# Optimization experiments

Measured on AMD Instinct MI355X. Metric: run time of the kernel, lower is better.

The kernel has to match this reference:

```python
import jax, jax.numpy as jnp
import numpy as np

K = 5          # kernel_size per pseudo-coordinate dim
N_NODES = 50000
N_EDGES = 800000
N_GRAPHS = 128


def _spline_basis(pseudo):
    # degree-1 open B-spline basis in 2-D pseudo coordinates.
    v = jnp.clip(pseudo, 0.0, 1.0) * (K - 1)            # [E,2]
    k0 = jnp.clip(jnp.floor(v), 0, K - 2).astype(jnp.int32)  # [E,2]
    frac = v - k0.astype(v.dtype)                        # [E,2]
    return k0, frac


def _spline_conv(x, src, dst, k0, frac, weight, root, bias, n_nodes):
    # weight: [K*K, in, out]. Precompute per-node per-kernel transform
    # to avoid materializing per-edge [E,in,out] weights.
    x_k = jnp.einsum('ni,kio->nko', x, weight)           # [N, 25, out]
    out_dim = weight.shape[2]
    msg = jnp.zeros((src.shape[0], out_dim), dtype=x.dtype)
    for b0 in range(2):          # 2^dim = 4 contributing basis combos
        for b1 in range(2):
            basis = ((frac[:, 0] if b0 else 1.0 - frac[:, 0])
                     * (frac[:, 1] if b1 else 1.0 - frac[:, 1]))   # [E]
            idx = (k0[:, 0] + b0) * K + (k0[:, 1] + b1)            # [E]
            msg = msg + basis[:, None] * x_k[src, idx]             # gather [E,out]
    agg = jax.ops.segment_sum(msg, dst, num_segments=n_nodes)      # [N,out]
    deg = jax.ops.segment_sum(jnp.ones((src.shape[0],), x.dtype), dst,
                              num_segments=n_nodes)
    agg = agg / jnp.maximum(deg, 1.0)[:, None]                     # aggr='mean'
    return agg + x @ root + bias


def setup_inputs() -> dict:
    key = jax.random.key(0)
    ks = jax.random.split(key, 16)
    x = jax.random.normal(ks[0], (N_NODES, 8), dtype=jnp.float32)
    edge_index = jax.random.randint(ks[1], (2, N_EDGES), 0, N_NODES, dtype=jnp.int32)
    pseudo = jax.random.uniform(ks[2], (N_EDGES, 2), dtype=jnp.float32)
    batch = jnp.sort(jax.random.randint(ks[3], (N_NODES,), 0, N_GRAPHS, dtype=jnp.int32))
    s = 0.1
    w1 = s * jax.random.normal(ks[4], (K * K, 8, 32), dtype=jnp.float32)
    r1 = s * jax.random.normal(ks[5], (8, 32), dtype=jnp.float32)
    b1 = jnp.zeros((32,), jnp.float32)
    w2 = s * jax.random.normal(ks[6], (K * K, 32, 64), dtype=jnp.float32)
    r2 = s * jax.random.normal(ks[7], (32, 64), dtype=jnp.float32)
    b2 = jnp.zeros((64,), jnp.float32)
    w3 = s * jax.random.normal(ks[8], (K * K, 64, 64), dtype=jnp.float32)
    r3 = s * jax.random.normal(ks[9], (64, 64), dtype=jnp.float32)
    b3 = jnp.zeros((64,), jnp.float32)
    fc_w = s * jax.random.normal(ks[10], (64, 30), dtype=jnp.float32)
    fc_b = jnp.zeros((30,), jnp.float32)
    return dict(x=x, edge_index=edge_index, pseudo=pseudo, batch=batch,
                w1=w1, r1=r1, b1=b1, w2=w2, r2=r2, b2=b2, w3=w3, r3=r3, b3=b3,
                fc_w=fc_w, fc_b=fc_b)


def reference(x, edge_index, pseudo, batch, w1, r1, b1, w2, r2, b2, w3, r3, b3, fc_w, fc_b):
    src, dst = edge_index[0], edge_index[1]
    k0, frac = _spline_basis(pseudo)
    h = jax.nn.elu(_spline_conv(x, src, dst, k0, frac, w1, r1, b1, N_NODES))
    h = jax.nn.elu(_spline_conv(h, src, dst, k0, frac, w2, r2, b2, N_NODES))
    h = jax.nn.elu(_spline_conv(h, src, dst, k0, frac, w3, r3, b3, N_NODES))
    # scatter_mean pooling over graphs (data.batch)
    pooled = jax.ops.segment_sum(h, batch, num_segments=N_GRAPHS)
    cnt = jax.ops.segment_sum(jnp.ones((N_NODES,), h.dtype), batch,
                              num_segments=N_GRAPHS)
    pooled = pooled / jnp.maximum(cnt, 1.0)[:, None]     # [G,64]
    # dropout is identity at inference
    logits = pooled @ fc_w + fc_b                        # [G,30]
    return jax.nn.log_softmax(logits, axis=1)
```

## Files before the change

### kernel.cpp

```cpp
#include <hip/hip_runtime.h>
#include <hip/hip_bf16.h>
#include <math.h>


typedef __attribute__((ext_vector_type(8))) short bf16x8;
typedef __attribute__((ext_vector_type(4))) float f32x4;

constexpr int SCAN_CHUNK = 2048;

__device__ __forceinline__ unsigned short f2bf(float f) {
    union { float f; unsigned u; } v; v.f = f;
    return (unsigned short)((v.u + 0x7fffu + ((v.u >> 16) & 1u)) >> 16);
}
__device__ __forceinline__ float bf2f(unsigned short h) {
    union { unsigned u; float f; } v; v.u = ((unsigned)h) << 16;
    return v.f;
}
__device__ __forceinline__ int pairaddr(int kk) {
    int slice = kk >> 5;
    return (slice >> 1) * 72 + (slice & 1) * 32 + (kk & 31);
}


__global__ void hist_kernel(const int* __restrict__ ei, int* __restrict__ deg, int E) {
    int e = blockIdx.x * blockDim.x + threadIdx.x;
    if (e < E) atomicAdd(&deg[ei[E + e]], 1);
}

__global__ __launch_bounds__(256) void scan1_kernel(const int* __restrict__ deg,
                                                    int* __restrict__ blockSums, int n) {
    __shared__ int wsum[4];
    int tid = threadIdx.x, lane = tid & 63, wave = tid >> 6;
    int idx0 = blockIdx.x * SCAN_CHUNK + tid * 8;
    int s = 0;
    #pragma unroll
    for (int u = 0; u < 8; ++u) {
        int id = idx0 + u;
        int d = (id < n) ? deg[id] : 0;
        s += (d + 7) & ~7;
    }
    #pragma unroll
    for (int off = 1; off < 64; off <<= 1) s += __shfl_xor(s, off);
    if (lane == 0) wsum[wave] = s;
    __syncthreads();
    if (tid == 0) blockSums[blockIdx.x] = wsum[0] + wsum[1] + wsum[2] + wsum[3];
}

__global__ void scan2_kernel(int* __restrict__ blockSums, int* __restrict__ row_start,
                             int nb, int n) {
    int lane = threadIdx.x & 63;
    int v = (lane < nb) ? blockSums[lane] : 0;
    int inc = v;
    #pragma unroll
    for (int off = 1; off < 64; off <<= 1) {
        int t = __shfl_up(inc, off);
        if (lane >= off) inc += t;
    }
    if (lane < nb) blockSums[lane] = inc - v;
    if (lane == 63) row_start[n] = inc;
}

__global__ __launch_bounds__(256) void scan3_kernel(const int* __restrict__ deg,
                                                    const int* __restrict__ blockSums,
                                                    int* __restrict__ row_start,
                                                    int* __restrict__ cursor,
                                                    float* __restrict__ invdeg, int n) {
    __shared__ int wsum[4];
    int tid = threadIdx.x, lane = tid & 63, wave = tid >> 6;
    int carry = blockSums[blockIdx.x];
    int idx0 = blockIdx.x * SCAN_CHUNK + tid * 8;
    int v[8], pre[8];
    int s = 0;
    #pragma unroll
    for (int u = 0; u < 8; ++u) {
        int id = idx0 + u;
        int d = (id < n) ? deg[id] : 0;
        v[u] = d;
        pre[u] = s;
        s += (d + 7) & ~7;
    }
    int inc = s;
    #pragma unroll
    for (int off = 1; off < 64; off <<= 1) {
        int t = __shfl_up(inc, off);
        if (lane >= off) inc += t;
    }
    if (lane == 63) wsum[wave] = inc;
    __syncthreads();
    int woff = 0;
    for (int w2 = 0; w2 < wave; ++w2) woff += wsum[w2];
    int eb = carry + woff + inc - s;
    #pragma unroll
    for (int u = 0; u < 8; ++u) {
        int id = idx0 + u;
        if (id < n) {
            int rs = eb + pre[u];
            row_start[id] = rs;
            cursor[id] = rs;
            invdeg[id] = 1.0f / fmaxf((float)v[u], 1.0f);
        }
    }
}

__global__ void scatter_kernel(const int* __restrict__ ei, const float* __restrict__ pseudo,
                               const float* __restrict__ invdeg, int* __restrict__ cursor,
                               uint2* __restrict__ basisB, unsigned* __restrict__ metaB, int E) {
    int e = blockIdx.x * blockDim.x + threadIdx.x;
    if (e >= E) return;
    int src = ei[e], dst = ei[E + e];
    float p0 = pseudo[2 * e], p1 = pseudo[2 * e + 1];
    float v0 = fminf(fmaxf(p0, 0.f), 1.f) * 4.f;
    float v1 = fminf(fmaxf(p1, 0.f), 1.f) * 4.f;
    int k00 = min((int)floorf(v0), 3);
    int k01 = min((int)floorf(v1), 3);
    float f0 = v0 - (float)k00, f1 = v1 - (float)k01;
    float g0 = 1.f - f0, g1 = 1.f - f1;
    float sc = invdeg[dst];
    int i00 = k00 * 5 + k01;
    int pos = atomicAdd(&cursor[dst], 1);
    uint2 b;
    b.x = (unsigned)f2bf(g0 * g1 * sc) | ((unsigned)f2bf(g0 * f1 * sc) << 16);
    b.y = (unsigned)f2bf(f0 * g1 * sc) | ((unsigned)f2bf(f0 * f1 * sc) << 16);
    basisB[pos] = b;
    metaB[pos] = (unsigned)src | ((unsigned)i00 << 20);
}

template <int Cin, int Cout, int KW>
__global__ void wprep_kernel(const float* __restrict__ W, const float* __restrict__ root,
                             unsigned short* __restrict__ WtF) {
    constexpr int NT = Cout / 16;
    int idx = blockIdx.x * 256 + threadIdx.x;
    if (idx >= Cout * KW) return;
    int e = idx & 7;
    int lane = (idx >> 3) & 63;
    int sn = idx >> 9;
    int s = sn / NT, nt = sn - s * NT;
    int r16 = lane & 15, g8 = lane >> 4;
    int o = nt * 16 + r16;
    int kk = s * 32 + g8 * 8 + e;
    float v = 0.f;
    if (kk < 26 * Cin) {
        int k = kk / Cin, i = kk - k * Cin;
        v = (k < 25) ? W[(k * Cin + i) * Cout + o] : root[i * Cout + o];
    }
    WtF[idx] = f2bf(v);
}


template <int Cin, int Cout, bool F32IN>
__global__ __launch_bounds__(512, 4) void layer_kernel(
        const void* __restrict__ xin_, const unsigned short* __restrict__ WtF,
        const float* __restrict__ bias, const int* __restrict__ row_start,
        const int* __restrict__ row_end, const uint2* __restrict__ basisG,
        const unsigned* __restrict__ metaG, unsigned short* __restrict__ xout,
        int nNodes) {
    constexpr int T = 16;
    constexpr int SLICES = (26 * Cin + 31) / 32;
    constexpr int NPAIR = (SLICES + 1) / 2;
    constexpr int ST = NPAIR * 72 + 8;
    constexpr int MT = (Cin + 15) / 16;
    constexpr int NT_B = Cout / 16;
    constexpr int W8 = 8 / NT_B;
    constexpr int RS = Cout + 4;
    constexpr int BSZ = 32 * 34;
    constexpr int DEPTH = (MT <= 2) ? 2 : 1;

    __shared__ __align__(16) unsigned short acc[T * ST];
    __shared__ __align__(16) unsigned short Ball[8 * BSZ];

    const int tid = threadIdx.x;
    const int node0 = blockIdx.x * T;
    const int wave = tid >> 6, lane = tid & 63;
    const int r16 = lane & 15, g8 = lane >> 4;
    const float* xf = (const float*)xin_;
    const unsigned short* xb = (const unsigned short*)xin_;

    {
        uint4 z = make_uint4(0u, 0u, 0u, 0u);
        for (int p = tid; p < T * ST / 8; p += 512) ((uint4*)acc)[p] = z;
    }
    __syncthreads();
    for (int p = tid; p < T * Cin; p += 512) {
        int t = p / Cin, i = p - t * Cin;
        int n = node0 + t;
        if (n < nNodes) {
            unsigned short v = F32IN ? f2bf(xf[n * Cin + i]) : xb[n * Cin + i];
            acc[t * ST + pairaddr(25 * Cin + i)] = v;
        }
    }

    unsigned short* Bw = Ball + wave * BSZ;
    {
        const int t0 = wave, t1 = wave + 8;
        const int na = node0 + t0, nb = node0 + t1;
        int eb0 = 0, ee0 = 0, eb1 = 0, ee1 = 0;
        if (na < nNodes) { eb0 = row_start[na]; ee0 = row_end[na]; }
        if (nb < nNodes) { eb1 = row_start[nb]; ee1 = row_end[nb]; }
        const int nc0 = (ee0 - eb0 + 31) >> 5;
        const int nc1 = (ee1 - eb1 + 31) >> 5;
        const int TC = nc0 + nc1;

        if (TC > 0) {
            auto info = [&](int vc, int& base, int& ee) {
                bool first = vc < nc0;
                int c = first ? vc : vc - nc0;
                base = (first ? eb0 : eb1) + (c << 5);
                ee = first ? ee0 : ee1;
            };
            auto loadMeta = [&](int vc, uint4& a, uint4& b) {
                int base, ee;
                info(vc, base, ee);
                const uint4* p = (const uint4*)(metaG + base + g8 * 8);
                a = p[0];
                b = p[1];
            };
            auto gatherA = [&](const uint4& a, const uint4& b, bf16x8* af) {
                int s[8];
                s[0] = a.x & 0xFFFFF; s[1] = a.y & 0xFFFFF;
                s[2] = a.z & 0xFFFFF; s[3] = a.w & 0xFFFFF;
                s[4] = b.x & 0xFFFFF; s[5] = b.y & 0xFFFFF;
                s[6] = b.z & 0xFFFFF; s[7] = b.w & 0xFFFFF;
                #pragma unroll
                for (int mt = 0; mt < MT; ++mt) {
                    int col = (Cin >= 16) ? (mt * 16 + r16) : (r16 & (Cin - 1));
                    #pragma unroll
                    for (int j = 0; j < 8; ++j)
                        af[mt][j] = (short)(F32IN ? f2bf(xf[s[j] * Cin + col])
                                                  : xb[s[j] * Cin + col]);
                }
            };
            auto loadScat = [&](int vc, unsigned& bx, unsigned& by, int& i00,
                                bool& valid) {
                int base, ee;
                info(vc, base, ee);
                int e = base + (lane & 31);
                valid = (lane < 32) && (e < ee);
                uint2 bb = basisG[e];
                unsigned mm = metaG[e];
                bx = bb.x;
                by = bb.y;
                i00 = (int)(mm >> 20);
            };

            f32x4 d[MT][2];
            #pragma unroll
            for (int mt = 0; mt < MT; ++mt)
                #pragma unroll
                for (int nt = 0; nt < 2; ++nt)
                    d[mt][nt] = (f32x4){0.f, 0.f, 0.f, 0.f};

            auto spill = [&](int t) {
                #pragma unroll
                for (int nt = 0; nt < 2; ++nt) {
                    int k = nt * 16 + r16;
                    if (k < 25) {
                        #pragma unroll
                        for (int mt = 0; mt < MT; ++mt) {
                            int ch0 = mt * 16 + g8 * 4;
                            if (ch0 < Cin) {
                                unsigned p0 = (unsigned)f2bf(d[mt][nt][0]) |
                                              ((unsigned)f2bf(d[mt][nt][1]) << 16);
                                unsigned p1 = (unsigned)f2bf(d[mt][nt][2]) |
                                              ((unsigned)f2bf(d[mt][nt][3]) << 16);
                                *(uint2*)&acc[t * ST + pairaddr(k * Cin + ch0)] =
                                    make_uint2(p0, p1);
                            }
                        }
                    }
                }
                #pragma unroll
                for (int mt = 0; mt < MT; ++mt)
                    #pragma unroll
                    for (int nt = 0; nt < 2; ++nt)
                        d[mt][nt] = (f32x4){0.f, 0.f, 0.f, 0.f};
            };

            auto computeB = [&](unsigned bxC, unsigned byC, int i00C, bool vldC,
                                bf16x8* af) {
                uint4 z = make_uint4(0u, 0u, 0u, 0u);
                uint4* b4 = (uint4*)Bw;
                #pragma unroll
                for (int q = 0; q < 3; ++q) {
                    int p = lane + q * 64;
                    if (p < BSZ / 8) b4[p] = z;
                }
                if (vldC) {
                    int le = lane & 31;
                    Bw[le * 34 + i00C]     = (unsigned short)(bxC & 0xFFFFu);
                    Bw[le * 34 + i00C + 1] = (unsigned short)(bxC >> 16);
                    Bw[le * 34 + i00C + 5] = (unsigned short)(byC & 0xFFFFu);
                    Bw[le * 34 + i00C + 6] = (unsigned short)(byC >> 16);
                }
                #pragma unroll
                for (int nt = 0; nt < 2; ++nt) {
                    bf16x8 bfr;
                    #pragma unroll
                    for (int j = 0; j < 8; ++j)
                        bfr[j] = (short)Bw[(g8 * 8 + j) * 34 + nt * 16 + r16];
                    #pragma unroll
                    for (int mt = 0; mt < MT; ++mt)
                        d[mt][nt] = __builtin_amdgcn_mfma_f32_16x16x32_bf16(
                            af[mt], bfr, d[mt][nt], 0, 0, 0);
                }
            };

            if constexpr (DEPTH == 2) {
                uint4 m2a, m2b;
                bf16x8 af0[MT], af1[MT], af2[MT];
                unsigned bxC, byC, bxN, byN;
                int i00C, i00N;
                bool vldC, vldN;
                {
                    uint4 a, b;
                    loadMeta(0, a, b);
                    gatherA(a, b, af0);
                    if (TC > 1) {
                        loadMeta(1, a, b);
                        gatherA(a, b, af1);
                    }
                    if (TC > 2) loadMeta(2, m2a, m2b);
                }
                loadScat(0, bxC, byC, i00C, vldC);

                for (int vc = 0; vc < TC; ++vc) {
                    if (vc + 2 < TC) {
                        gatherA(m2a, m2b, af2);
                        if (vc + 3 < TC) loadMeta(vc + 3, m2a, m2b);
                    }
                    if (vc + 1 < TC) loadScat(vc + 1, bxN, byN, i00N, vldN);

                    computeB(bxC, byC, i00C, vldC, af0);
                    if (vc == nc0 - 1) spill(t0);

                    #pragma unroll
                    for (int mt = 0; mt < MT; ++mt) {
                        af0[mt] = af1[mt];
                        af1[mt] = af2[mt];
                    }
                    bxC = bxN; byC = byN; i00C = i00N; vldC = vldN;
                }
                if (nc1 > 0) spill(t1);
            } else {
                uint4 nA, nB;
                bf16x8 afC[MT], afN[MT];
                unsigned bxC, byC, bxN, byN;
                int i00C, i00N;
                bool vldC, vldN;
                {
                    uint4 a, b;
                    loadMeta(0, a, b);
                    gatherA(a, b, afC);
                }
                loadScat(0, bxC, byC, i00C, vldC);
                if (TC > 1) loadMeta(1, nA, nB);

                for (int vc = 0; vc < TC; ++vc) {
                    if (vc + 1 < TC) {
                        gatherA(nA, nB, afN);
                        if (vc + 2 < TC) loadMeta(vc + 2, nA, nB);
                        loadScat(vc + 1, bxN, byN, i00N, vldN);
                    }

                    computeB(bxC, byC, i00C, vldC, afC);
                    if (vc == nc0 - 1) spill(t0);

                    #pragma unroll
                    for (int mt = 0; mt < MT; ++mt) afC[mt] = afN[mt];
                    bxC = bxN; byC = byN; i00C = i00N; vldC = vldN;
                }
                if (nc1 > 0) spill(t1);
            }
        }
    }
    __syncthreads();

    const int q = wave / NT_B;
    const int nt = wave % NT_B;
    f32x4 db = {0.f, 0.f, 0.f, 0.f};
    {
        const unsigned short* ap = acc + r16 * ST;
        for (int s = q; s < SLICES; s += W8) {
            bf16x8 a8 = *(const bf16x8*)(ap + (s >> 1) * 72 + (s & 1) * 32 + g8 * 8);
            bf16x8 b8 = *(const bf16x8*)(WtF + ((size_t)(s * NT_B + nt) * 64 + lane) * 8);
            db = __builtin_amdgcn_mfma_f32_16x16x32_bf16(a8, b8, db, 0, 0, 0);
        }
    }
    __syncthreads();
    float* red = (float*)acc;
    if (q > 0) {
        #pragma unroll
        for (int j = 0; j < 4; ++j)
            red[((q - 1) * T + g8 * 4 + j) * RS + nt * 16 + r16] = db[j];
    }
    __syncthreads();
    if (q == 0) {
        const int o = nt * 16 + r16;
        const float bo = bias[o];
        #pragma unroll
        for (int j = 0; j < 4; ++j) {
            int row = g8 * 4 + j;
            int n = node0 + row;
            if (n < nNodes) {
                float v = db[j] + bo;
                #pragma unroll
                for (int q2 = 1; q2 < W8; ++q2)
                    v += red[((q2 - 1) * T + row) * RS + o];
                v = (v > 0.f) ? v : expm1f(v);
                xout[n * Cout + o] = f2bf(v);
            }
        }
    }
}


__global__ void pool_kernel(const unsigned short* __restrict__ h, const int* __restrict__ batch,
                            float* __restrict__ pooled, float* __restrict__ cnt, int n) {
    int gw = (blockIdx.x * blockDim.x + threadIdx.x) >> 6;
    int lane = threadIdx.x & 63;
    int nw = (gridDim.x * blockDim.x) >> 6;
    int per = (n + nw - 1) / nw;
    int n0 = gw * per, n1 = min(n0 + per, n);
    if (n0 >= n1) return;
    int cur = batch[n0];
    float s = 0.f, c = 0.f;
    for (int nn = n0; nn < n1; ++nn) {
        int g = batch[nn];
        if (g != cur) {
            atomicAdd(&pooled[cur * 64 + lane], s);
            if (lane == 0) atomicAdd(&cnt[cur], c);
            s = 0.f; c = 0.f; cur = g;
        }
        s += bf2f(h[nn * 64 + lane]);
        c += 1.f;
    }
    atomicAdd(&pooled[cur * 64 + lane], s);
    if (lane == 0) atomicAdd(&cnt[cur], c);
}

__global__ __launch_bounds__(128) void head_kernel(const float* __restrict__ pooled,
                                                   const float* __restrict__ cnt,
                                                   const float* __restrict__ fcw,
                                                   const float* __restrict__ fcb,
                                                   float* __restrict__ outp, int G) {
    int g = threadIdx.x;
    if (g >= G) return;
    float inv = 1.f / fmaxf(cnt[g], 1.f);
    float l[30];
    float m = -1e30f;
    #pragma unroll
    for (int j = 0; j < 30; ++j) {
        float s = fcb[j];
        for (int i = 0; i < 64; ++i) s += pooled[g * 64 + i] * inv * fcw[i * 30 + j];
        l[j] = s;
        m = fmaxf(m, s);
    }
    float lse = 0.f;
    #pragma unroll
    for (int j = 0; j < 30; ++j) lse += expf(l[j] - m);
    lse = logf(lse);
    #pragma unroll
    for (int j = 0; j < 30; ++j) outp[g * 30 + j] = l[j] - m - lse;
}


extern "C" void kernel_launch(void* const* d_in, const int* in_sizes, int n_in,
                              void* d_out, int out_size, void* d_ws, size_t ws_size,
                              hipStream_t stream) {
    const float* x = (const float*)d_in[0];
    const int* ei = (const int*)d_in[1];
    const float* ps = (const float*)d_in[2];
    const int* batch = (const int*)d_in[3];
    const float *w1 = (const float*)d_in[4], *r1 = (const float*)d_in[5], *b1 = (const float*)d_in[6];
    const float *w2 = (const float*)d_in[7], *r2 = (const float*)d_in[8], *b2 = (const float*)d_in[9];
    const float *w3 = (const float*)d_in[10], *r3 = (const float*)d_in[11], *b3 = (const float*)d_in[12];
    const float *fcw = (const float*)d_in[13], *fcb = (const float*)d_in[14];
    float* outp = (float*)d_out;

    const int nN = in_sizes[0] / 8;
    const int E = in_sizes[1] / 2;
    const int G = out_size / 30;
    const int EP = E + 8 * nN + 64;
    const int NSB = (nN + SCAN_CHUNK - 1) / SCAN_CHUNK;

    char* wsb = (char*)d_ws;
    size_t off = 0;
    auto alloc = [&](size_t b) -> char* {
        char* p = wsb + off;
        off = (off + b + 255) & ~(size_t)255;
        return p;
    };
    int* deg = (int*)alloc((size_t)nN * 4);
    int* row_start = (int*)alloc((size_t)(nN + 1) * 4);
    int* cursor = (int*)alloc((size_t)nN * 4);
    float* invdeg = (float*)alloc((size_t)nN * 4);
    int* blockSums = (int*)alloc((size_t)64 * 4);
    uint2* basisB = (uint2*)alloc((size_t)EP * 8);
    unsigned* metaB = (unsigned*)alloc((size_t)EP * 4);
    unsigned short* wt1 = (unsigned short*)alloc((size_t)32 * 224 * 2);
    unsigned short* wt2 = (unsigned short*)alloc((size_t)64 * 832 * 2);
    unsigned short* wt3 = (unsigned short*)alloc((size_t)64 * 1664 * 2);
    unsigned short* h1 = (unsigned short*)alloc((size_t)nN * 32 * 2);
    unsigned short* h2 = (unsigned short*)alloc((size_t)nN * 64 * 2);
    unsigned short* h3 = (unsigned short*)alloc((size_t)nN * 64 * 2);
    float* pooled = (float*)alloc((size_t)G * 64 * 4);
    float* cnt = (float*)alloc((size_t)G * 4);
    (void)ws_size;

    hipMemsetAsync(deg, 0, (size_t)nN * 4, stream);
    hipMemsetAsync(metaB, 0, (size_t)EP * 4, stream);
    hipMemsetAsync(pooled, 0, (size_t)G * 64 * 4, stream);
    hipMemsetAsync(cnt, 0, (size_t)G * 4, stream);

    int ebk = (E + 255) / 256;
    hist_kernel<<<ebk, 256, 0, stream>>>(ei, deg, E);
    scan1_kernel<<<NSB, 256, 0, stream>>>(deg, blockSums, nN);
    scan2_kernel<<<1, 64, 0, stream>>>(blockSums, row_start, NSB, nN);
    scan3_kernel<<<NSB, 256, 0, stream>>>(deg, blockSums, row_start, cursor, invdeg, nN);
    scatter_kernel<<<ebk, 256, 0, stream>>>(ei, ps, invdeg, cursor, basisB, metaB, E);
    wprep_kernel<8, 32, 224><<<(32 * 224 + 255) / 256, 256, 0, stream>>>(w1, r1, wt1);
    wprep_kernel<32, 64, 832><<<(64 * 832 + 255) / 256, 256, 0, stream>>>(w2, r2, wt2);
    wprep_kernel<64, 64, 1664><<<(64 * 1664 + 255) / 256, 256, 0, stream>>>(w3, r3, wt3);

    int nb = (nN + 15) / 16;
    layer_kernel<8, 32, true><<<nb, 512, 0, stream>>>(
        x, wt1, b1, row_start, cursor, basisB, metaB, h1, nN);
    layer_kernel<32, 64, false><<<nb, 512, 0, stream>>>(
        h1, wt2, b2, row_start, cursor, basisB, metaB, h2, nN);
    layer_kernel<64, 64, false><<<nb, 512, 0, stream>>>(
        h2, wt3, b3, row_start, cursor, basisB, metaB, h3, nN);

    pool_kernel<<<128, 256, 0, stream>>>(h3, batch, pooled, cnt, nN);
    head_kernel<<<1, 128, 0, stream>>>(pooled, cnt, fcw, fcb, outp, G);
}
```

Before: 373.8 us.

## Interleave hidden feature layout so edge gathers load multiple channels per access

Intermediate bf16 node features are stored in a permuted, channel-interleaved order so that each lane's channels for all M-tiles sit next to each other. The per-edge gather can then fetch 2 or 4 bf16 values with one 32- or 64-bit load instead of several scalar 16-bit loads. The root-term staging, the output store and the pooling/head indexing are remapped to match the permuted layout. This cuts the number of memory instructions in the dominant gather path, but the output stores become strided and the layout bookkeeping spans several kernels.

```diff
diff --git a/kernel.cpp b/kernel.cpp
--- a/kernel.cpp
+++ b/kernel.cpp
@@ -181,11 +181,15 @@
     }
     __syncthreads();
     for (int p = tid; p < T * Cin; p += 512) {
-        int t = p / Cin, i = p - t * Cin;
+        int t = p / Cin, pp = p - t * Cin;
         int n = node0 + t;
         if (n < nNodes) {
-            unsigned short v = F32IN ? f2bf(xf[n * Cin + i]) : xb[n * Cin + i];
-            acc[t * ST + pairaddr(25 * Cin + i)] = v;
+            if constexpr (F32IN) {
+                acc[t * ST + pairaddr(25 * Cin + pp)] = f2bf(xf[n * Cin + pp]);
+            } else {
+                int i = (pp % MT) * 16 + pp / MT;
+                acc[t * ST + pairaddr(25 * Cin + i)] = xb[n * Cin + pp];
+            }
         }
     }
 
@@ -220,13 +224,26 @@
                 s[2] = a.z & 0xFFFFF; s[3] = a.w & 0xFFFFF;
                 s[4] = b.x & 0xFFFFF; s[5] = b.y & 0xFFFFF;
                 s[6] = b.z & 0xFFFFF; s[7] = b.w & 0xFFFFF;
-                #pragma unroll
-                for (int mt = 0; mt < MT; ++mt) {
-                    int col = (Cin >= 16) ? (mt * 16 + r16) : (r16 & (Cin - 1));
+                if constexpr (F32IN) {
                     #pragma unroll
                     for (int j = 0; j < 8; ++j)
-                        af[mt][j] = (short)(F32IN ? f2bf(xf[s[j] * Cin + col])
-                                                  : xb[s[j] * Cin + col]);
+                        af[0][j] = (short)f2bf(xf[s[j] * Cin + (r16 & (Cin - 1))]);
+                } else if constexpr (MT == 4) {
+                    #pragma unroll
+                    for (int j = 0; j < 8; ++j) {
+                        uint2 w = *(const uint2*)(xb + (size_t)s[j] * Cin + r16 * 4);
+                        af[0][j] = (short)(unsigned short)(w.x & 0xFFFFu);
+                        af[1][j] = (short)(unsigned short)(w.x >> 16);
+                        af[2][j] = (short)(unsigned short)(w.y & 0xFFFFu);
+                        af[3][j] = (short)(unsigned short)(w.y >> 16);
+                    }
+                } else {
+                    #pragma unroll
+                    for (int j = 0; j < 8; ++j) {
+                        unsigned w = *(const unsigned*)(xb + (size_t)s[j] * Cin + r16 * 2);
+                        af[0][j] = (short)(unsigned short)(w & 0xFFFFu);
+                        af[1][j] = (short)(unsigned short)(w >> 16);
+                    }
                 }
             };
             auto loadScat = [&](int vc, unsigned& bx, unsigned& by, int& i00,
@@ -406,7 +423,7 @@
                 for (int q2 = 1; q2 < W8; ++q2)
                     v += red[((q2 - 1) * T + row) * RS + o];
                 v = (v > 0.f) ? v : expm1f(v);
-                xout[n * Cout + o] = f2bf(v);
+                xout[n * Cout + r16 * NT_B + nt] = f2bf(v);
             }
         }
     }
@@ -450,7 +467,10 @@
     #pragma unroll
     for (int j = 0; j < 30; ++j) {
         float s = fcb[j];
-        for (int i = 0; i < 64; ++i) s += pooled[g * 64 + i] * inv * fcw[i * 30 + j];
+        for (int i = 0; i < 64; ++i) {
+            int p = (i & 15) * 4 + (i >> 4);
+            s += pooled[g * 64 + p] * inv * fcw[i * 30 + j];
+        }
         l[j] = s;
         m = fmaxf(m, s);
     }
```

After: 436.1 us. +16.7%, slower.
